# Kernel optimization log

Measured on AMD Instinct MI355X. Metric: run time of the kernel, lower is better.

The kernel has to match this reference:

```python
import jax, jax.numpy as jnp
import numpy as np
from jax import lax

BS, N = 64, 16384
SEG_NUM_ALL = 16
NUM_FPS = 256


def setup_inputs() -> dict:
    key = jax.random.key(0)
    k_pts, k_lab = jax.random.split(key)
    pts = jax.random.normal(k_pts, (BS, N, 3), dtype=jnp.float32)
    label = jax.random.randint(k_lab, (BS, N), 0, SEG_NUM_ALL).astype(jnp.float32)
    x = jnp.concatenate([pts, label[..., None]], axis=-1)  # [BS, N, 4]
    return {"x": x}


def _masked_fps(pts, mask):
    """Farthest-point sampling of NUM_FPS points from pts[mask].
    pts: [N,3] float, mask: [N] bool. Starts from the first valid point
    (matching pointnet2-style fps which starts at index 0 of the subset).
    Invalid points can never be selected (score forced to -inf).
    """
    start = jnp.argmax(mask)  # index of first True
    neg_inf = jnp.array(-jnp.inf, dtype=pts.dtype)
    init_d = jnp.full((pts.shape[0],), jnp.inf, dtype=pts.dtype)

    def step(carry, _):
        min_d, cur = carry
        cur_pt = pts[cur]                      # [3]
        d = jnp.sum((pts - cur_pt) ** 2, -1)   # [N] squared dist to newest pick
        min_d = jnp.minimum(min_d, d)
        nxt = jnp.argmax(jnp.where(mask, min_d, neg_inf))
        return (min_d, nxt), cur_pt

    _, sel = lax.scan(step, (init_d, start), None, length=NUM_FPS)
    return sel  # [NUM_FPS, 3]


def reference(x):
    points = x[..., :3]                 # [BS, N, 3]
    label = x[..., 3]                   # [BS, N]
    seg_ids = jnp.arange(SEG_NUM_ALL, dtype=label.dtype)
    seg_mask = label[:, None, :] == seg_ids[None, :, None]   # [BS, S, N] bool
    counts = seg_mask.sum(-1)                                 # [BS, S]
    masks = counts >= NUM_FPS                                 # [BS, S] bool

    # vmap over segments then over batch
    fps_segs = jax.vmap(lambda p, ms: jax.vmap(lambda m: _masked_fps(p, m))(ms))
    sel = fps_segs(points, seg_mask)                          # [BS, S, NUM_FPS, 3]

    group_points = jnp.where(masks[..., None, None], sel, jnp.zeros((), sel.dtype))
    return group_points, masks
```

## Files before the change

kernel.cpp:

```cpp
#include <hip/hip_runtime.h>
#include <math.h>

#define BSZ 64
#define NPT 16384
#define SEG 16
#define NFPS 256
#define MAXPTS 2048
#define NLANES 64

typedef __attribute__((ext_vector_type(2))) float f32x2;

__device__ __forceinline__ f32x2 pk_add(f32x2 a, f32x2 b) {
    f32x2 d;
    asm("v_pk_add_f32 %0, %1, %2" : "=v"(d) : "v"(a), "v"(b));
    return d;
}
__device__ __forceinline__ f32x2 pk_mul(f32x2 a, f32x2 b) {
    f32x2 d;
    asm("v_pk_mul_f32 %0, %1, %2" : "=v"(d) : "v"(a), "v"(b));
    return d;
}

template <int CTRL>
__device__ __forceinline__ float dpp_max_f32(float v) {
    const int o = __builtin_amdgcn_update_dpp(0, __float_as_int(v), CTRL, 0xf, 0xf, true);
    return fmaxf(v, __int_as_float(o));
}

template <int P>
__device__ __forceinline__ void fps_phase2(const float4* __restrict__ pts,
                                           float* __restrict__ out,
                                           size_t gp_base, int count, int lane) {
    f32x2 xp[P], yp[P], zp[P];
    float md[2 * P];
    #pragma unroll
    for (int p = 0; p < P; ++p) {
        const int i0 = (2 * p) * NLANES + lane;
        const int i1 = i0 + NLANES;
        const bool v0 = (i0 < count), v1 = (i1 < count);
        const float4 q0 = pts[v0 ? i0 : 0];
        const float4 q1 = pts[v1 ? i1 : 0];
        xp[p].x = q0.x; xp[p].y = q1.x;
        yp[p].x = q0.y; yp[p].y = q1.y;
        zp[p].x = q0.z; zp[p].y = q1.z;
        md[2 * p]     = v0 ? INFINITY : -INFINITY;
        md[2 * p + 1] = v1 ? INFINITY : -INFINITY;
    }

    float4 c = pts[0];
    for (int t = 0; t < NFPS; ++t) {
        if (lane < 3)
            out[gp_base + (size_t)t * 3 + lane] = (lane == 0) ? c.x : ((lane == 1) ? c.y : c.z);

        f32x2 ncx; ncx.x = -c.x; ncx.y = -c.x;
        f32x2 ncy; ncy.x = -c.y; ncy.y = -c.y;
        f32x2 ncz; ncz.x = -c.z; ncz.y = -c.z;

        float a0 = -INFINITY, a1 = -INFINITY, a2 = -INFINITY, a3 = -INFINITY;
        #pragma unroll
        for (int p = 0; p < P; ++p) {
            const f32x2 dx = pk_add(xp[p], ncx);
            const f32x2 dy = pk_add(yp[p], ncy);
            const f32x2 dz = pk_add(zp[p], ncz);
            const f32x2 d = pk_add(pk_add(pk_mul(dx, dx), pk_mul(dy, dy)), pk_mul(dz, dz));
            const float m0 = fminf(md[2 * p], d.x);
            const float m1 = fminf(md[2 * p + 1], d.y);
            md[2 * p] = m0;
            md[2 * p + 1] = m1;
            if (p & 1) { a2 = fmaxf(a2, m0); a3 = fmaxf(a3, m1); }
            else       { a0 = fmaxf(a0, m0); a1 = fmaxf(a1, m1); }
        }
        float best = fmaxf(fmaxf(a0, a1), fmaxf(a2, a3));

        best = dpp_max_f32<0x111>(best);
        best = dpp_max_f32<0x112>(best);
        best = dpp_max_f32<0x114>(best);
        best = dpp_max_f32<0x118>(best);
        best = dpp_max_f32<0x142>(best);
        best = dpp_max_f32<0x143>(best);
        const float wv = __int_as_float(__builtin_amdgcn_readlane(__float_as_int(best), 63));

        int mslot = 0x7fff;
        #pragma unroll
        for (int sl = 2 * P - 1; sl >= 0; --sl)
            if (md[sl] == wv) mslot = sl;

        const unsigned long long wm = __ballot(mslot != 0x7fff);
        const int winlane = __builtin_amdgcn_readfirstlane(__ffsll((long long)wm) - 1);
        const int wslot = __builtin_amdgcn_readlane(mslot, winlane);
        c = pts[wslot * NLANES + winlane];
    }
}

__global__ __launch_bounds__(NLANES, 1) void fps_part_kernel(const float* __restrict__ x,
                                                             float* __restrict__ out) {
    const int blk = blockIdx.x;
    const int xcd = blk & 7;
    const int grp = blk >> 3;
    const int b = (xcd << 3) | (grp >> 4);
    const int s = grp & 15;
    const int prob = b * SEG + s;
    const int lane = threadIdx.x;

    __shared__ float4 pts[MAXPTS];

    const float4* x4 = (const float4*)x + (size_t)b * NPT;
    const float fs = (float)s;
    const unsigned long long lanemask = (1ull << lane) - 1ull;
    int total = 0;

    for (int mc = 0; mc < 32; ++mc) {
        float4 p[8];
        #pragma unroll
        for (int j = 0; j < 8; ++j)
            p[j] = x4[(mc * 8 + j) * NLANES + lane];
        #pragma unroll
        for (int j = 0; j < 8; ++j) {
            const bool pred = (p[j].w == fs);
            const unsigned long long m = __ballot(pred);
            const int pos = total + __popcll(m & lanemask);
            if (pred && pos < MAXPTS) pts[pos] = p[j];
            total += __popcll(m);
        }
    }
    __syncthreads();

    const int count = (total < MAXPTS) ? total : MAXPTS;
    const size_t gp_base = (size_t)prob * NFPS * 3;
    const size_t mask_off = (size_t)BSZ * SEG * NFPS * 3 + (size_t)prob;

    if (count < NFPS) {
        for (int i = lane; i < NFPS * 3; i += NLANES) out[gp_base + i] = 0.0f;
        if (lane == 0) out[mask_off] = 0.0f;
        return;
    }
    if (lane == 0) out[mask_off] = 1.0f;

    const int cnt_s = __builtin_amdgcn_readfirstlane(count);
    const int pmax = (cnt_s + 127) >> 7;

    if (pmax <= 8)       fps_phase2<8>(pts, out, gp_base, count, lane);
    else if (pmax == 9)  fps_phase2<9>(pts, out, gp_base, count, lane);
    else                 fps_phase2<16>(pts, out, gp_base, count, lane);
}

extern "C" void kernel_launch(void* const* d_in, const int* in_sizes, int n_in,
                              void* d_out, int out_size, void* d_ws, size_t ws_size,
                              hipStream_t stream) {
    const float* x = (const float*)d_in[0];
    float* out = (float*)d_out;
    fps_part_kernel<<<BSZ * SEG, NLANES, 0, stream>>>(x, out);
}
```

Baseline: 257.8 us.

## Split each FPS problem across two waves with per-iteration LDS argmax exchange

Each block now uses two wavefronts. Each wave compacts the matching points from half of the point cloud into its own region of shared memory, then runs farthest-point sampling on its half. The two waves combine their per-iteration maxima through a double-buffered shared-memory exchange and a __syncthreads. This halves the per-wave register working set and per-iteration distance work, which allows smaller template sizes and two blocks per CU. In exchange it adds a block barrier every iteration. The slot search is also split into four independent min chains to shorten the dependency chain. Ties between the two waves resolve to wave 0, which may pick a different point than the reference when distances are exactly equal.

```diff
diff --git a/kernel.cpp b/kernel.cpp
--- a/kernel.cpp
+++ b/kernel.cpp
@@ -5,8 +5,9 @@
 #define NPT 16384
 #define SEG 16
 #define NFPS 256
-#define MAXPTS 2048
+#define RCAP 1024
 #define NLANES 64
+#define NTHREADS 128
 
 typedef __attribute__((ext_vector_type(2))) float f32x2;
 
@@ -29,17 +30,19 @@
 
 template <int P>
 __device__ __forceinline__ void fps_phase2(const float4* __restrict__ pts,
-                                           float* __restrict__ out,
-                                           size_t gp_base, int count, int lane) {
+                                           float* __restrict__ out, size_t gp_base,
+                                           int cw, int wave, int lane, int start_idx,
+                                           volatile float* xv, volatile int* xi) {
+    const int rbase = wave * RCAP;
     f32x2 xp[P], yp[P], zp[P];
     float md[2 * P];
     #pragma unroll
     for (int p = 0; p < P; ++p) {
         const int i0 = (2 * p) * NLANES + lane;
         const int i1 = i0 + NLANES;
-        const bool v0 = (i0 < count), v1 = (i1 < count);
-        const float4 q0 = pts[v0 ? i0 : 0];
-        const float4 q1 = pts[v1 ? i1 : 0];
+        const bool v0 = (i0 < cw), v1 = (i1 < cw);
+        const float4 q0 = pts[rbase + (v0 ? i0 : 0)];
+        const float4 q1 = pts[rbase + (v1 ? i1 : 0)];
         xp[p].x = q0.x; xp[p].y = q1.x;
         yp[p].x = q0.y; yp[p].y = q1.y;
         zp[p].x = q0.z; zp[p].y = q1.z;
@@ -47,9 +50,9 @@
         md[2 * p + 1] = v1 ? INFINITY : -INFINITY;
     }
 
-    float4 c = pts[0];
+    float4 c = pts[start_idx];
     for (int t = 0; t < NFPS; ++t) {
-        if (lane < 3)
+        if (wave == 0 && lane < 3)
             out[gp_base + (size_t)t * 3 + lane] = (lane == 0) ? c.x : ((lane == 1) ? c.y : c.z);
 
         f32x2 ncx; ncx.x = -c.x; ncx.y = -c.x;
@@ -80,36 +83,57 @@
         best = dpp_max_f32<0x143>(best);
         const float wv = __int_as_float(__builtin_amdgcn_readlane(__float_as_int(best), 63));
 
-        int mslot = 0x7fff;
+        int mc0 = 0x7fff, mc1 = 0x7fff, mc2 = 0x7fff, mc3 = 0x7fff;
         #pragma unroll
-        for (int sl = 2 * P - 1; sl >= 0; --sl)
-            if (md[sl] == wv) mslot = sl;
+        for (int sl = 2 * P - 1; sl >= 0; --sl) {
+            const bool hit = (md[sl] == wv);
+            switch (sl & 3) {
+                case 0: mc0 = hit ? sl : mc0; break;
+                case 1: mc1 = hit ? sl : mc1; break;
+                case 2: mc2 = hit ? sl : mc2; break;
+                case 3: mc3 = hit ? sl : mc3; break;
+            }
+        }
+        const int ms = min(min(mc0, mc1), min(mc2, mc3));
 
-        const unsigned long long wm = __ballot(mslot != 0x7fff);
-        const int winlane = __builtin_amdgcn_readfirstlane(__ffsll((long long)wm) - 1);
-        const int wslot = __builtin_amdgcn_readlane(mslot, winlane);
-        c = pts[wslot * NLANES + winlane];
+        const unsigned long long bm = __ballot(ms != 0x7fff);
+        const int wl = __builtin_amdgcn_readfirstlane(__ffsll((long long)bm) - 1);
+        const int wsl = __builtin_amdgcn_readlane(ms, wl & 63);
+        const int idx = rbase + wsl * NLANES + (wl & 63);
+        const float wvv = (cw == 0) ? -INFINITY : wv;
+
+        const int buf = t & 1;
+        if (lane == 0) { xv[buf * 2 + wave] = wvv; xi[buf * 2 + wave] = idx; }
+        __syncthreads();
+        const float v0 = xv[buf * 2 + 0], v1 = xv[buf * 2 + 1];
+        const int j0 = xi[buf * 2 + 0], j1 = xi[buf * 2 + 1];
+        c = pts[(v1 > v0) ? j1 : j0];
     }
 }
 
-__global__ __launch_bounds__(NLANES, 1) void fps_part_kernel(const float* __restrict__ x,
-                                                             float* __restrict__ out) {
+__global__ __launch_bounds__(NTHREADS, 2) void fps_part_kernel(const float* __restrict__ x,
+                                                               float* __restrict__ out) {
     const int blk = blockIdx.x;
     const int xcd = blk & 7;
     const int grp = blk >> 3;
     const int b = (xcd << 3) | (grp >> 4);
     const int s = grp & 15;
     const int prob = b * SEG + s;
-    const int lane = threadIdx.x;
+    const int tid = threadIdx.x;
+    const int lane = tid & 63;
+    const int wave = tid >> 6;
 
-    __shared__ float4 pts[MAXPTS];
+    __shared__ float4 pts[2 * RCAP];
+    __shared__ int cnt_sh[2];
+    __shared__ float xv[4];
+    __shared__ int xi[4];
 
-    const float4* x4 = (const float4*)x + (size_t)b * NPT;
+    const float4* x4 = (const float4*)x + (size_t)b * NPT + wave * (NPT / 2);
     const float fs = (float)s;
     const unsigned long long lanemask = (1ull << lane) - 1ull;
     int total = 0;
 
-    for (int mc = 0; mc < 32; ++mc) {
+    for (int mc = 0; mc < 16; ++mc) {
         float4 p[8];
         #pragma unroll
         for (int j = 0; j < 8; ++j)
@@ -119,29 +143,35 @@
             const bool pred = (p[j].w == fs);
             const unsigned long long m = __ballot(pred);
             const int pos = total + __popcll(m & lanemask);
-            if (pred && pos < MAXPTS) pts[pos] = p[j];
+            if (pred && pos < RCAP) pts[wave * RCAP + pos] = p[j];
             total += __popcll(m);
         }
     }
+    const int cw = (total < RCAP) ? total : RCAP;
+    if (lane == 0) cnt_sh[wave] = cw;
     __syncthreads();
+    const int c0 = cnt_sh[0], c1 = cnt_sh[1];
+    const int count = c0 + c1;
 
-    const int count = (total < MAXPTS) ? total : MAXPTS;
     const size_t gp_base = (size_t)prob * NFPS * 3;
     const size_t mask_off = (size_t)BSZ * SEG * NFPS * 3 + (size_t)prob;
 
     if (count < NFPS) {
-        for (int i = lane; i < NFPS * 3; i += NLANES) out[gp_base + i] = 0.0f;
-        if (lane == 0) out[mask_off] = 0.0f;
+        for (int i = tid; i < NFPS * 3; i += NTHREADS) out[gp_base + i] = 0.0f;
+        if (tid == 0) out[mask_off] = 0.0f;
         return;
     }
-    if (lane == 0) out[mask_off] = 1.0f;
+    if (tid == 0) out[mask_off] = 1.0f;
 
-    const int cnt_s = __builtin_amdgcn_readfirstlane(count);
-    const int pmax = (cnt_s + 127) >> 7;
+    const int start_idx = (c0 > 0) ? 0 : RCAP;
+    const int cmx = (c0 > c1) ? c0 : c1;
+    const int pmax = (__builtin_amdgcn_readfirstlane(cmx) + 127) >> 7;
 
-    if (pmax <= 8)       fps_phase2<8>(pts, out, gp_base, count, lane);
-    else if (pmax == 9)  fps_phase2<9>(pts, out, gp_base, count, lane);
-    else                 fps_phase2<16>(pts, out, gp_base, count, lane);
+    if (pmax <= 4)      fps_phase2<4>(pts, out, gp_base, cw, wave, lane, start_idx, xv, xi);
+    else if (pmax == 5) fps_phase2<5>(pts, out, gp_base, cw, wave, lane, start_idx, xv, xi);
+    else if (pmax == 6) fps_phase2<6>(pts, out, gp_base, cw, wave, lane, start_idx, xv, xi);
+    else if (pmax <= 8) fps_phase2<8>(pts, out, gp_base, cw, wave, lane, start_idx, xv, xi);
+    else                fps_phase2<16>(pts, out, gp_base, cw, wave, lane, start_idx, xv, xi);
 }
 
 extern "C" void kernel_launch(void* const* d_in, const int* in_sizes, int n_in,
@@ -149,5 +179,5 @@
                               hipStream_t stream) {
     const float* x = (const float*)d_in[0];
     float* out = (float*)d_out;
-    fps_part_kernel<<<BSZ * SEG, NLANES, 0, stream>>>(x, out);
+    fps_part_kernel<<<BSZ * SEG, NTHREADS, 0, stream>>>(x, out);
 }
```

Result: slower. 302.4 us (+17.3%).

## Process two segments per wavefront with interleaved dual FPS chains

Applied to the files above, without the earlier changes.

Each block now compacts and runs farthest-point sampling for two segments at once, sharing one scan of the batch's points and interleaving the two independent argmax chains within a single wave. This halves the redundant global reads of the point cloud and exposes instruction-level parallelism across the latency-bound reduction steps. In exchange, it halves the block count, doubles register use and per-wave ALU work, and may leave SIMDs idle. It also adds a pmax==10 specialization.

```diff
diff --git a/kernel.cpp b/kernel.cpp
--- a/kernel.cpp
+++ b/kernel.cpp
@@ -5,7 +5,7 @@
 #define NPT 16384
 #define SEG 16
 #define NFPS 256
-#define MAXPTS 2048
+#define RCAP 2048
 #define NLANES 64
 
 typedef __attribute__((ext_vector_type(2))) float f32x2;
@@ -28,67 +28,108 @@
 }
 
 template <int P>
-__device__ __forceinline__ void fps_phase2(const float4* __restrict__ pts,
-                                           float* __restrict__ out,
-                                           size_t gp_base, int count, int lane) {
-    f32x2 xp[P], yp[P], zp[P];
-    float md[2 * P];
+__device__ __forceinline__ void fps2_dual(const float4* __restrict__ pts,
+                                          float* __restrict__ out,
+                                          size_t gpA, size_t gpB,
+                                          int cA, int cB, bool vA, bool vB, int lane) {
+    f32x2 xA[P], yA[P], zA[P], xB[P], yB[P], zB[P];
+    float mdA[2 * P], mdB[2 * P];
     #pragma unroll
     for (int p = 0; p < P; ++p) {
         const int i0 = (2 * p) * NLANES + lane;
         const int i1 = i0 + NLANES;
-        const bool v0 = (i0 < count), v1 = (i1 < count);
-        const float4 q0 = pts[v0 ? i0 : 0];
-        const float4 q1 = pts[v1 ? i1 : 0];
-        xp[p].x = q0.x; xp[p].y = q1.x;
-        yp[p].x = q0.y; yp[p].y = q1.y;
-        zp[p].x = q0.z; zp[p].y = q1.z;
-        md[2 * p]     = v0 ? INFINITY : -INFINITY;
-        md[2 * p + 1] = v1 ? INFINITY : -INFINITY;
-    }
-
-    float4 c = pts[0];
+        const bool a0 = (i0 < cA), a1 = (i1 < cA);
+        const bool b0 = (i0 < cB), b1 = (i1 < cB);
+        const float4 qa0 = pts[a0 ? i0 : 0];
+        const float4 qa1 = pts[a1 ? i1 : 0];
+        const float4 qb0 = pts[RCAP + (b0 ? i0 : 0)];
+        const float4 qb1 = pts[RCAP + (b1 ? i1 : 0)];
+        xA[p].x = qa0.x; xA[p].y = qa1.x; yA[p].x = qa0.y; yA[p].y = qa1.y;
+        zA[p].x = qa0.z; zA[p].y = qa1.z;
+        xB[p].x = qb0.x; xB[p].y = qb1.x; yB[p].x = qb0.y; yB[p].y = qb1.y;
+        zB[p].x = qb0.z; zB[p].y = qb1.z;
+        mdA[2 * p] = a0 ? INFINITY : -INFINITY;
+        mdA[2 * p + 1] = a1 ? INFINITY : -INFINITY;
+        mdB[2 * p] = b0 ? INFINITY : -INFINITY;
+        mdB[2 * p + 1] = b1 ? INFINITY : -INFINITY;
+    }
+
+    float4 ca = pts[0];
+    float4 cb = pts[RCAP];
     for (int t = 0; t < NFPS; ++t) {
-        if (lane < 3)
-            out[gp_base + (size_t)t * 3 + lane] = (lane == 0) ? c.x : ((lane == 1) ? c.y : c.z);
-
-        f32x2 ncx; ncx.x = -c.x; ncx.y = -c.x;
-        f32x2 ncy; ncy.x = -c.y; ncy.y = -c.y;
-        f32x2 ncz; ncz.x = -c.z; ncz.y = -c.z;
+        if (vA && lane < 3)
+            out[gpA + (size_t)t * 3 + lane] = (lane == 0) ? ca.x : ((lane == 1) ? ca.y : ca.z);
+        if (vB && lane >= 32 && lane < 35)
+            out[gpB + (size_t)t * 3 + (lane - 32)] =
+                (lane == 32) ? cb.x : ((lane == 33) ? cb.y : cb.z);
+
+        f32x2 nax; nax.x = -ca.x; nax.y = -ca.x;
+        f32x2 nay; nay.x = -ca.y; nay.y = -ca.y;
+        f32x2 naz; naz.x = -ca.z; naz.y = -ca.z;
+        f32x2 nbx; nbx.x = -cb.x; nbx.y = -cb.x;
+        f32x2 nby; nby.x = -cb.y; nby.y = -cb.y;
+        f32x2 nbz; nbz.x = -cb.z; nbz.y = -cb.z;
 
         float a0 = -INFINITY, a1 = -INFINITY, a2 = -INFINITY, a3 = -INFINITY;
+        float b0 = -INFINITY, b1 = -INFINITY, b2 = -INFINITY, b3 = -INFINITY;
         #pragma unroll
         for (int p = 0; p < P; ++p) {
-            const f32x2 dx = pk_add(xp[p], ncx);
-            const f32x2 dy = pk_add(yp[p], ncy);
-            const f32x2 dz = pk_add(zp[p], ncz);
-            const f32x2 d = pk_add(pk_add(pk_mul(dx, dx), pk_mul(dy, dy)), pk_mul(dz, dz));
-            const float m0 = fminf(md[2 * p], d.x);
-            const float m1 = fminf(md[2 * p + 1], d.y);
-            md[2 * p] = m0;
-            md[2 * p + 1] = m1;
-            if (p & 1) { a2 = fmaxf(a2, m0); a3 = fmaxf(a3, m1); }
-            else       { a0 = fmaxf(a0, m0); a1 = fmaxf(a1, m1); }
+            const f32x2 dxa = pk_add(xA[p], nax);
+            const f32x2 dya = pk_add(yA[p], nay);
+            const f32x2 dza = pk_add(zA[p], naz);
+            const f32x2 da = pk_add(pk_add(pk_mul(dxa, dxa), pk_mul(dya, dya)), pk_mul(dza, dza));
+            const float ma0 = fminf(mdA[2 * p], da.x);
+            const float ma1 = fminf(mdA[2 * p + 1], da.y);
+            mdA[2 * p] = ma0; mdA[2 * p + 1] = ma1;
+            if (p & 1) { a2 = fmaxf(a2, ma0); a3 = fmaxf(a3, ma1); }
+            else       { a0 = fmaxf(a0, ma0); a1 = fmaxf(a1, ma1); }
+
+            const f32x2 dxb = pk_add(xB[p], nbx);
+            const f32x2 dyb = pk_add(yB[p], nby);
+            const f32x2 dzb = pk_add(zB[p], nbz);
+            const f32x2 db = pk_add(pk_add(pk_mul(dxb, dxb), pk_mul(dyb, dyb)), pk_mul(dzb, dzb));
+            const float mb0 = fminf(mdB[2 * p], db.x);
+            const float mb1 = fminf(mdB[2 * p + 1], db.y);
+            mdB[2 * p] = mb0; mdB[2 * p + 1] = mb1;
+            if (p & 1) { b2 = fmaxf(b2, mb0); b3 = fmaxf(b3, mb1); }
+            else       { b0 = fmaxf(b0, mb0); b1 = fmaxf(b1, mb1); }
         }
-        float best = fmaxf(fmaxf(a0, a1), fmaxf(a2, a3));
-
-        best = dpp_max_f32<0x111>(best);
-        best = dpp_max_f32<0x112>(best);
-        best = dpp_max_f32<0x114>(best);
-        best = dpp_max_f32<0x118>(best);
-        best = dpp_max_f32<0x142>(best);
-        best = dpp_max_f32<0x143>(best);
-        const float wv = __int_as_float(__builtin_amdgcn_readlane(__float_as_int(best), 63));
-
-        int mslot = 0x7fff;
-        #pragma unroll
-        for (int sl = 2 * P - 1; sl >= 0; --sl)
-            if (md[sl] == wv) mslot = sl;
-
-        const unsigned long long wm = __ballot(mslot != 0x7fff);
-        const int winlane = __builtin_amdgcn_readfirstlane(__ffsll((long long)wm) - 1);
-        const int wslot = __builtin_amdgcn_readlane(mslot, winlane);
-        c = pts[wslot * NLANES + winlane];
+        float bestA = fmaxf(fmaxf(a0, a1), fmaxf(a2, a3));
+        float bestB = fmaxf(fmaxf(b0, b1), fmaxf(b2, b3));
+
+        bestA = dpp_max_f32<0x111>(bestA); bestB = dpp_max_f32<0x111>(bestB);
+        bestA = dpp_max_f32<0x112>(bestA); bestB = dpp_max_f32<0x112>(bestB);
+        bestA = dpp_max_f32<0x114>(bestA); bestB = dpp_max_f32<0x114>(bestB);
+        bestA = dpp_max_f32<0x118>(bestA); bestB = dpp_max_f32<0x118>(bestB);
+        bestA = dpp_max_f32<0x142>(bestA); bestB = dpp_max_f32<0x142>(bestB);
+        bestA = dpp_max_f32<0x143>(bestA); bestB = dpp_max_f32<0x143>(bestB);
+        const float wvA = __int_as_float(__builtin_amdgcn_readlane(__float_as_int(bestA), 63));
+        const float wvB = __int_as_float(__builtin_amdgcn_readlane(__float_as_int(bestB), 63));
+
+        int ac0 = 0x7fff, ac1 = 0x7fff, ac2 = 0x7fff, ac3 = 0x7fff;
+        int bc0 = 0x7fff, bc1 = 0x7fff, bc2 = 0x7fff, bc3 = 0x7fff;
+        #pragma unroll
+        for (int sl = 2 * P - 1; sl >= 0; --sl) {
+            const bool ha = (mdA[sl] == wvA);
+            const bool hb = (mdB[sl] == wvB);
+            switch (sl & 3) {
+                case 0: ac0 = ha ? sl : ac0; bc0 = hb ? sl : bc0; break;
+                case 1: ac1 = ha ? sl : ac1; bc1 = hb ? sl : bc1; break;
+                case 2: ac2 = ha ? sl : ac2; bc2 = hb ? sl : bc2; break;
+                case 3: ac3 = ha ? sl : ac3; bc3 = hb ? sl : bc3; break;
+            }
+        }
+        const int msA = min(min(ac0, ac1), min(ac2, ac3));
+        const int msB = min(min(bc0, bc1), min(bc2, bc3));
+
+        const unsigned long long bmA = __ballot(msA != 0x7fff);
+        const unsigned long long bmB = __ballot(msB != 0x7fff);
+        const int wlA = __builtin_amdgcn_readfirstlane(__ffsll((long long)bmA) - 1);
+        const int wlB = __builtin_amdgcn_readfirstlane(__ffsll((long long)bmB) - 1);
+        const int wslA = min(__builtin_amdgcn_readlane(msA, wlA & 63), 2 * P - 1);
+        const int wslB = min(__builtin_amdgcn_readlane(msB, wlB & 63), 2 * P - 1);
+        ca = pts[wslA * NLANES + (wlA & 63)];
+        cb = pts[RCAP + wslB * NLANES + (wlB & 63)];
     }
 }
 
@@ -97,17 +138,18 @@
     const int blk = blockIdx.x;
     const int xcd = blk & 7;
     const int grp = blk >> 3;
-    const int b = (xcd << 3) | (grp >> 4);
-    const int s = grp & 15;
-    const int prob = b * SEG + s;
+    const int b = (xcd << 3) | (grp >> 3);
+    const int sp = grp & 7;
+    const int s0 = 2 * sp, s1 = 2 * sp + 1;
+    const int probA = b * SEG + s0;
+    const int probB = b * SEG + s1;
     const int lane = threadIdx.x;
 
-    __shared__ float4 pts[MAXPTS];
+    __shared__ float4 pts[2 * RCAP];
 
     const float4* x4 = (const float4*)x + (size_t)b * NPT;
-    const float fs = (float)s;
-    const unsigned long long lanemask = (1ull << lane) - 1ull;
-    int total = 0;
+    const float fsA = (float)s0, fsB = (float)s1;
+    int tA = 0, tB = 0;
 
     for (int mc = 0; mc < 32; ++mc) {
         float4 p[8];
@@ -116,32 +158,44 @@
             p[j] = x4[(mc * 8 + j) * NLANES + lane];
         #pragma unroll
         for (int j = 0; j < 8; ++j) {
-            const bool pred = (p[j].w == fs);
-            const unsigned long long m = __ballot(pred);
-            const int pos = total + __popcll(m & lanemask);
-            if (pred && pos < MAXPTS) pts[pos] = p[j];
-            total += __popcll(m);
+            const bool prA = (p[j].w == fsA);
+            const bool prB = (p[j].w == fsB);
+            const unsigned long long mA = __ballot(prA);
+            const unsigned long long mB = __ballot(prB);
+            const int posA = tA + __builtin_amdgcn_mbcnt_hi((unsigned)(mA >> 32),
+                                  __builtin_amdgcn_mbcnt_lo((unsigned)mA, 0));
+            const int posB = tB + __builtin_amdgcn_mbcnt_hi((unsigned)(mB >> 32),
+                                  __builtin_amdgcn_mbcnt_lo((unsigned)mB, 0));
+            if (prA && posA < RCAP) pts[posA] = p[j];
+            if (prB && posB < RCAP) pts[RCAP + posB] = p[j];
+            tA += __popcll(mA);
+            tB += __popcll(mB);
         }
     }
     __syncthreads();
 
-    const int count = (total < MAXPTS) ? total : MAXPTS;
-    const size_t gp_base = (size_t)prob * NFPS * 3;
-    const size_t mask_off = (size_t)BSZ * SEG * NFPS * 3 + (size_t)prob;
-
-    if (count < NFPS) {
-        for (int i = lane; i < NFPS * 3; i += NLANES) out[gp_base + i] = 0.0f;
-        if (lane == 0) out[mask_off] = 0.0f;
-        return;
-    }
-    if (lane == 0) out[mask_off] = 1.0f;
-
-    const int cnt_s = __builtin_amdgcn_readfirstlane(count);
-    const int pmax = (cnt_s + 127) >> 7;
-
-    if (pmax <= 8)       fps_phase2<8>(pts, out, gp_base, count, lane);
-    else if (pmax == 9)  fps_phase2<9>(pts, out, gp_base, count, lane);
-    else                 fps_phase2<16>(pts, out, gp_base, count, lane);
+    const int cA = (tA < RCAP) ? tA : RCAP;
+    const int cB = (tB < RCAP) ? tB : RCAP;
+    const bool vA = (cA >= NFPS), vB = (cB >= NFPS);
+    const size_t gpA = (size_t)probA * NFPS * 3;
+    const size_t gpB = (size_t)probB * NFPS * 3;
+    const size_t maskbase = (size_t)BSZ * SEG * NFPS * 3;
+
+    if (lane == 0) {
+        out[maskbase + probA] = vA ? 1.0f : 0.0f;
+        out[maskbase + probB] = vB ? 1.0f : 0.0f;
+    }
+    if (!vA) for (int i = lane; i < NFPS * 3; i += NLANES) out[gpA + i] = 0.0f;
+    if (!vB) for (int i = lane; i < NFPS * 3; i += NLANES) out[gpB + i] = 0.0f;
+    if (!vA && !vB) return;
+
+    const int cmx = (cA > cB) ? cA : cB;
+    const int pmax = (__builtin_amdgcn_readfirstlane(cmx) + 127) >> 7;
+
+    if (pmax <= 8)       fps2_dual<8>(pts, out, gpA, gpB, cA, cB, vA, vB, lane);
+    else if (pmax == 9)  fps2_dual<9>(pts, out, gpA, gpB, cA, cB, vA, vB, lane);
+    else if (pmax == 10) fps2_dual<10>(pts, out, gpA, gpB, cA, cB, vA, vB, lane);
+    else                 fps2_dual<16>(pts, out, gpA, gpB, cA, cB, vA, vB, lane);
 }
 
 extern "C" void kernel_launch(void* const* d_in, const int* in_sizes, int n_in,
@@ -149,5 +203,5 @@
                               hipStream_t stream) {
     const float* x = (const float*)d_in[0];
     float* out = (float*)d_out;
-    fps_part_kernel<<<BSZ * SEG, NLANES, 0, stream>>>(x, out);
-}
+    fps_part_kernel<<<BSZ * SEG / 2, NLANES, 0, stream>>>(x, out);
+}
```

New measurement: 385.5 us. +49.6%, slower.

## Fuse argmax index into packed 64-bit key reduction and batch output stores

Applied to the files above, without the earlier changes.

Each lane now tracks the argmax slot alongside its max value and packs value and inverted index into a 64-bit key. A single DPP max reduction then yields both the winning distance and its point index, which removes the post-reduction slot scan, ballot and second readlane. The selected centers are buffered in registers per lane and written out after the loop, replacing the per-iteration global stores. In exchange each DPP step now moves two 32-bit halves and does a 64-bit compare, the inner loop gains compare/select work for index tracking, and register pressure rises.

```diff
diff --git a/kernel.cpp b/kernel.cpp
--- a/kernel.cpp
+++ b/kernel.cpp
@@ -22,9 +22,11 @@
 }
 
 template <int CTRL>
-__device__ __forceinline__ float dpp_max_f32(float v) {
-    const int o = __builtin_amdgcn_update_dpp(0, __float_as_int(v), CTRL, 0xf, 0xf, true);
-    return fmaxf(v, __int_as_float(o));
+__device__ __forceinline__ unsigned long long dpp_max_u64(unsigned long long k) {
+    const int lo = __builtin_amdgcn_update_dpp(0, (int)(unsigned)k, CTRL, 0xf, 0xf, true);
+    const int hi = __builtin_amdgcn_update_dpp(0, (int)(unsigned)(k >> 32), CTRL, 0xf, 0xf, true);
+    const unsigned long long ok = ((unsigned long long)(unsigned)hi << 32) | (unsigned)lo;
+    return ok > k ? ok : k;
 }
 
 template <int P>
@@ -48,47 +50,74 @@
     }
 
     float4 c = pts[0];
-    for (int t = 0; t < NFPS; ++t) {
-        if (lane < 3)
-            out[gp_base + (size_t)t * 3 + lane] = (lane == 0) ? c.x : ((lane == 1) ? c.y : c.z);
+    float scx[4], scy[4], scz[4];
 
-        f32x2 ncx; ncx.x = -c.x; ncx.y = -c.x;
-        f32x2 ncy; ncy.x = -c.y; ncy.y = -c.y;
-        f32x2 ncz; ncz.x = -c.z; ncz.y = -c.z;
+    #pragma unroll
+    for (int c4 = 0; c4 < 4; ++c4) {
+        for (int tt = 0; tt < 64; ++tt) {
+            const bool mine = (lane == tt);
+            scx[c4] = mine ? c.x : scx[c4];
+            scy[c4] = mine ? c.y : scy[c4];
+            scz[c4] = mine ? c.z : scz[c4];
 
-        float a0 = -INFINITY, a1 = -INFINITY, a2 = -INFINITY, a3 = -INFINITY;
-        #pragma unroll
-        for (int p = 0; p < P; ++p) {
-            const f32x2 dx = pk_add(xp[p], ncx);
-            const f32x2 dy = pk_add(yp[p], ncy);
-            const f32x2 dz = pk_add(zp[p], ncz);
-            const f32x2 d = pk_add(pk_add(pk_mul(dx, dx), pk_mul(dy, dy)), pk_mul(dz, dz));
-            const float m0 = fminf(md[2 * p], d.x);
-            const float m1 = fminf(md[2 * p + 1], d.y);
-            md[2 * p] = m0;
-            md[2 * p + 1] = m1;
-            if (p & 1) { a2 = fmaxf(a2, m0); a3 = fmaxf(a3, m1); }
-            else       { a0 = fmaxf(a0, m0); a1 = fmaxf(a1, m1); }
+            f32x2 ncx; ncx.x = -c.x; ncx.y = -c.x;
+            f32x2 ncy; ncy.x = -c.y; ncy.y = -c.y;
+            f32x2 ncz; ncz.x = -c.z; ncz.y = -c.z;
+
+            float bv0 = -INFINITY, bv1 = -INFINITY, bv2 = -INFINITY, bv3 = -INFINITY;
+            int bs0 = 0, bs1 = 0, bs2 = 0, bs3 = 0;
+            #pragma unroll
+            for (int p = 0; p < P; ++p) {
+                const f32x2 dx = pk_add(xp[p], ncx);
+                const f32x2 dy = pk_add(yp[p], ncy);
+                const f32x2 dz = pk_add(zp[p], ncz);
+                const f32x2 d = pk_add(pk_add(pk_mul(dx, dx), pk_mul(dy, dy)),
+                                       pk_mul(dz, dz));
+                const float m0 = fminf(md[2 * p], d.x);
+                const float m1 = fminf(md[2 * p + 1], d.y);
+                md[2 * p] = m0;
+                md[2 * p + 1] = m1;
+                if (p & 1) {
+                    if (m0 > bv2) { bv2 = m0; bs2 = 2 * p; }
+                    if (m1 > bv3) { bv3 = m1; bs3 = 2 * p + 1; }
+                } else {
+                    if (m0 > bv0) { bv0 = m0; bs0 = 2 * p; }
+                    if (m1 > bv1) { bv1 = m1; bs1 = 2 * p + 1; }
+                }
+            }
+
+            const unsigned lo0 = ~(unsigned)((bs0 << 6) | lane);
+            const unsigned lo1 = ~(unsigned)((bs1 << 6) | lane);
+            const unsigned lo2 = ~(unsigned)((bs2 << 6) | lane);
+            const unsigned lo3 = ~(unsigned)((bs3 << 6) | lane);
+            unsigned long long k0 = ((unsigned long long)__float_as_uint(bv0) << 32) | lo0;
+            const unsigned long long k1 = ((unsigned long long)__float_as_uint(bv1) << 32) | lo1;
+            unsigned long long k2 = ((unsigned long long)__float_as_uint(bv2) << 32) | lo2;
+            const unsigned long long k3 = ((unsigned long long)__float_as_uint(bv3) << 32) | lo3;
+            if (k1 > k0) k0 = k1;
+            if (k3 > k2) k2 = k3;
+            unsigned long long key = (k2 > k0) ? k2 : k0;
+
+            key = dpp_max_u64<0x111>(key);
+            key = dpp_max_u64<0x112>(key);
+            key = dpp_max_u64<0x114>(key);
+            key = dpp_max_u64<0x118>(key);
+            key = dpp_max_u64<0x142>(key);
+            key = dpp_max_u64<0x143>(key);
+
+            const unsigned keylo =
+                (unsigned)__builtin_amdgcn_readlane((int)(unsigned)key, 63);
+            const int idx = (int)(~keylo);
+            c = pts[idx];
         }
-        float best = fmaxf(fmaxf(a0, a1), fmaxf(a2, a3));
+    }
 
-        best = dpp_max_f32<0x111>(best);
-        best = dpp_max_f32<0x112>(best);
-        best = dpp_max_f32<0x114>(best);
-        best = dpp_max_f32<0x118>(best);
-        best = dpp_max_f32<0x142>(best);
-        best = dpp_max_f32<0x143>(best);
-        const float wv = __int_as_float(__builtin_amdgcn_readlane(__float_as_int(best), 63));
-
-        int mslot = 0x7fff;
-        #pragma unroll
-        for (int sl = 2 * P - 1; sl >= 0; --sl)
-            if (md[sl] == wv) mslot = sl;
-
-        const unsigned long long wm = __ballot(mslot != 0x7fff);
-        const int winlane = __builtin_amdgcn_readfirstlane(__ffsll((long long)wm) - 1);
-        const int wslot = __builtin_amdgcn_readlane(mslot, winlane);
-        c = pts[wslot * NLANES + winlane];
+    #pragma unroll
+    for (int c4 = 0; c4 < 4; ++c4) {
+        const size_t o = gp_base + (size_t)(c4 * 64 + lane) * 3;
+        out[o + 0] = scx[c4];
+        out[o + 1] = scy[c4];
+        out[o + 2] = scz[c4];
     }
 }
 
```

After: 245.1 us. -4.9%, faster.
